# Kernel optimization log

Hardware: AMD Instinct MI355X
Metric: run time of the kernel (lower is better)

## Reference

```python
import jax, jax.numpy as jnp
import numpy as np

B = 4096          # batch_size
D_EMB = 16        # per-side embedding dim (embed_to_from width = 2*D_EMB)
D_HIGH = 784      # flattened high-dim feature size
NSR = 5           # negative_sample_rate
A = 1.576943      # UMAP _a
B_PARAM = 0.8950608  # UMAP _b
REPULSION = 1.0
EPS = 1e-4
GLOBAL_LOSS = 0.5
TOTAL_STEPS = 1000
BATCH_COUNT = 500  # fixed step for deterministic alpha/beta
WARMUP = int(0.05 * TOTAL_STEPS)


def _safe_sqrt(sq):
    # sqrt with zero (not NaN) gradient at 0, matching zero-distance pairs
    safe = jnp.where(sq > 0, sq, 1.0)
    return jnp.where(sq > 0, jnp.sqrt(safe), 0.0)


def _pairwise_dist(x):
    # ||x_i - x_j|| via gram trick; avoids materializing [N,N,D]
    sq = jnp.sum(x * x, axis=1)                      # [N]
    gram = x @ x.T                                   # [N,N]
    d2 = sq[:, None] + sq[None, :] - 2.0 * gram
    return _safe_sqrt(jnp.maximum(d2, 0.0))


def _umap_ce_loss(embed_to_from, perm):
    e_to, e_from = jnp.split(embed_to_from, 2, axis=1)   # [B, D_EMB] each
    neg_to = jnp.repeat(e_to, NSR, axis=0)               # [B*NSR, D_EMB]
    repeat_neg = jnp.repeat(e_from, NSR, axis=0)
    neg_from = repeat_neg[perm]                          # shuffled negatives
    d_pos = _safe_sqrt(jnp.sum((e_to - e_from) ** 2, axis=1))
    d_neg = _safe_sqrt(jnp.sum((neg_to - neg_from) ** 2, axis=1))
    dist = jnp.concatenate([d_pos, d_neg], axis=0)       # [B*(1+NSR)]
    p_dist = 1.0 / (1.0 + A * dist ** (2.0 * B_PARAM))
    p_graph = jnp.concatenate([jnp.ones(B, p_dist.dtype), jnp.zeros(B * NSR, p_dist.dtype)])
    attraction = -p_graph * jnp.log(jnp.clip(p_dist, EPS, 1.0))
    repellant = -(1.0 - p_graph) * jnp.log(jnp.clip(1.0 - p_dist, EPS, 1.0)) * REPULSION
    return jnp.mean(attraction + repellant)


def _global_feature_loss(embed_to_from, to_x):
    e_to = embed_to_from[:, :D_EMB]
    to_x = to_x.reshape(to_x.shape[0], -1)
    high_dis = _pairwise_dist(to_x)     # [N,N]
    low_dis = _pairwise_dist(e_to)      # [N,N]
    # row-wise pearson correlation between high_dis and low_dis
    h = high_dis - jnp.mean(high_dis, axis=1, keepdims=True)
    l = low_dis - jnp.mean(low_dis, axis=1, keepdims=True)
    num = jnp.sum(h * l, axis=1)
    den = jnp.sqrt(jnp.sum(h * h, axis=1)) * jnp.sqrt(jnp.sum(l * l, axis=1))
    corr = jnp.mean(num / den)
    return -corr


def _alpha_beta():
    if BATCH_COUNT >= WARMUP:
        if BATCH_COUNT <= 0.9 * TOTAL_STEPS:
            beta = max(0.0, GLOBAL_LOSS * (1 - BATCH_COUNT / (TOTAL_STEPS - WARMUP * 4)) ** 2)
        else:
            beta = 0.0
        alpha = max(0.0, 1 - beta)
    else:
        alpha = 0.0
        beta = GLOBAL_LOSS
    return alpha, beta


def setup_inputs() -> dict:
    key = jax.random.key(0)
    k1, k2, k3 = jax.random.split(key, 3)
    embed_to_from = jax.random.normal(k1, (B, 2 * D_EMB), dtype=jnp.float32)
    placeholder = jax.random.normal(k2, (B, D_HIGH), dtype=jnp.float32)
    perm = jax.random.permutation(k3, B * NSR).astype(jnp.int32)
    return {"embed_to_from": embed_to_from, "placeholder": placeholder, "perm": perm}


def reference(embed_to_from, placeholder, perm):
    loss = _umap_ce_loss(embed_to_from, perm)
    loss_g = _global_feature_loss(embed_to_from, placeholder)
    alpha, beta = _alpha_beta()
    return alpha * loss + beta * loss_g
```

## Files before the change

### kernel.cpp

```cpp
#include <hip/hip_runtime.h>
#include <hip/hip_bf16.h>
#include <math.h>

#define NB    4096
#define DH    784
#define KX8   832
#define NSR   5
#define NNEG  (NB*NSR)
#define NTOT  (NB + NNEG)

#define A_CONST 1.576943f
#define PEXP    1.7901216f
#define EPS_C   1.0e-4f
#define ALPHA_C 0.9296875f
#define BETA_C  0.0703125f

#define NBLK  528
#define BUFB  8192

typedef __hip_bfloat16 bf16;
typedef short bf16x8 __attribute__((ext_vector_type(8)));
typedef float f32x4  __attribute__((ext_vector_type(4)));
typedef float f32x2  __attribute__((ext_vector_type(2)));
typedef long long2v __attribute__((ext_vector_type(2)));

#define WS_XF8    0
#define WS_EBF    3407872
#define WS_SQX    3670016
#define WS_SQE    3686400
#define WS_ACC5   3702784
#define WS_UPART  8945664
#define WS_CNT    8946304

__device__ __forceinline__ void gl2lds16(const void* g, void* l) {
    __builtin_amdgcn_global_load_lds(
        (const __attribute__((address_space(1))) unsigned int*)g,
        (__attribute__((address_space(3))) unsigned int*)l,
        16, 0, 0);
}

__global__ void prep_fused(const float* __restrict__ X, const float* __restrict__ emb,
                           const int* __restrict__ perm, unsigned char* __restrict__ Xf8,
                           float* __restrict__ sqx, bf16* __restrict__ Ebf,
                           float* __restrict__ sqe, float* __restrict__ upart,
                           float* __restrict__ acc5, unsigned* __restrict__ cnt) {
    if (blockIdx.x == 0 && threadIdx.x == 0) *cnt = 0u;
    if (blockIdx.x < 1024) {
        const int wave = threadIdx.x >> 6, lane = threadIdx.x & 63;
        const int row = blockIdx.x * 4 + wave;
        const float4* xr = (const float4*)(X + (size_t)row * DH);
        int* xb = (int*)(Xf8 + (size_t)row * KX8);
        float s = 0.f;
        #pragma unroll
        for (int it = 0; it < 4; ++it) {
            const int idx = lane + it * 64;
            if (idx < 208) {
                const int c = idx >> 4, p = idx & 15;
                const int q = p >> 2, h = (p >> 1) & 1, w = p & 1;
                const int src = c * 16 + h * 8 + q * 2 + w;
                int pk = 0;
                if (src < 196) {
                    float4 v = xr[src];
                    s += v.x * v.x + v.y * v.y + v.z * v.z + v.w * v.w;
                    int lo = __builtin_amdgcn_cvt_pk_fp8_f32(v.x, v.y, 0, false);
                    pk = __builtin_amdgcn_cvt_pk_fp8_f32(v.z, v.w, lo, true);
                }
                xb[idx] = pk;
            }
        }
        #pragma unroll
        for (int off = 32; off; off >>= 1) s += __shfl_down(s, off, 64);
        if (lane == 0) sqx[row] = s;
        return;
    }
    const int ub = blockIdx.x - 1024;
    const int t = ub * 256 + threadIdx.x;
    if (t < 5 * NB) acc5[t] = 0.f;
    float val = 0.f;
    if (t < NB) {
        const float4* av = (const float4*)(emb + (size_t)t * 32);
        float4 t0 = av[0], t1 = av[1], t2 = av[2], t3 = av[3];
        float4 f0 = av[4], f1 = av[5], f2 = av[6], f3 = av[7];
        bf16* eb = Ebf + (size_t)t * 32;
        union { bf16 h[4]; ushort4 u; } cv;
        #define ST4(dst, q) cv.h[0]=__float2bfloat16(q.x); cv.h[1]=__float2bfloat16(q.y); \
                            cv.h[2]=__float2bfloat16(q.z); cv.h[3]=__float2bfloat16(q.w); \
                            *(ushort4*)(dst) = cv.u;
        ST4(eb,      t0) ST4(eb + 4,  t1) ST4(eb + 8,  t2) ST4(eb + 12, t3)
        #undef ST4
        ushort4 z = {0, 0, 0, 0};
        *(ushort4*)(eb + 16) = z; *(ushort4*)(eb + 20) = z;
        *(ushort4*)(eb + 24) = z; *(ushort4*)(eb + 28) = z;
        sqe[t] = t0.x*t0.x + t0.y*t0.y + t0.z*t0.z + t0.w*t0.w
               + t1.x*t1.x + t1.y*t1.y + t1.z*t1.z + t1.w*t1.w
               + t2.x*t2.x + t2.y*t2.y + t2.z*t2.z + t2.w*t2.w
               + t3.x*t3.x + t3.y*t3.y + t3.z*t3.z + t3.w*t3.w;
        float d2 = 0.f;
        #define D2(a, b) { float4 df = {a.x-b.x, a.y-b.y, a.z-b.z, a.w-b.w}; \
                           d2 += df.x*df.x + df.y*df.y + df.z*df.z + df.w*df.w; }
        D2(t0, f0) D2(t1, f1) D2(t2, f2) D2(t3, f3)
        #undef D2
        float d = sqrtf(d2);
        float p = 1.f / (1.f + A_CONST * powf(d, PEXP));
        val = -logf(fminf(fmaxf(p, EPS_C), 1.f));
    } else if (t < NTOT) {
        const int k = t - NB;
        const int ti = k / 5;
        const int fi = perm[k] / 5;
        const float4* at = (const float4*)(emb + (size_t)ti * 32);
        const float4* bt = (const float4*)(emb + (size_t)fi * 32 + 16);
        float d2 = 0.f;
        #pragma unroll
        for (int q = 0; q < 4; ++q) {
            float4 a = at[q], b = bt[q];
            float4 df = {a.x-b.x, a.y-b.y, a.z-b.z, a.w-b.w};
            d2 += df.x*df.x + df.y*df.y + df.z*df.z + df.w*df.w;
        }
        float d = sqrtf(d2);
        float p = 1.f / (1.f + A_CONST * powf(d, PEXP));
        val = -logf(fminf(fmaxf(1.f - p, EPS_C), 1.f));
    }
    #pragma unroll
    for (int off = 32; off; off >>= 1) val += __shfl_down(val, off, 64);
    __shared__ float ps[4];
    if ((threadIdx.x & 63) == 0) ps[threadIdx.x >> 6] = val;
    __syncthreads();
    if (threadIdx.x == 0) upart[ub] = ps[0] + ps[1] + ps[2] + ps[3];
}

__global__ __launch_bounds__(512, 4) void gram_kernel(
    const unsigned char* __restrict__ Xf8, const bf16* __restrict__ Ebf,
    const float* __restrict__ sqx, const float* __restrict__ sqe,
    float* __restrict__ acc5, const float* __restrict__ upart,
    unsigned* __restrict__ cnt, float* __restrict__ out) {
    __shared__ __align__(16) unsigned char smem[67584];
    unsigned char* As = smem;
    unsigned char* Bs = smem + 4 * BUFB;
    float* sqxs = (float*)(smem + 65536);
    float* sqes = (float*)(smem + 66560);
    float* scr  = (float*)smem;

#define BARLDS() do { asm volatile("s_waitcnt lgkmcnt(0)" ::: "memory"); \
                      __builtin_amdgcn_s_barrier(); } while (0)

    int bi, bj;
    {
        const int k = blockIdx.x & 7;
        const int idx = blockIdx.x >> 3;
        int g = -1, r = 0;
        if (k < 6) {
            const int SG[6] = {0,0,0,1,1,2}, SH[6] = {1,2,3,2,3,3};
            if (idx < 64) { bi = SG[k]*8 + (idx>>3); bj = SH[k]*8 + (idx&7); }
            else {
                const int DG[6] = {1,0,3,1,3,3};
                const int DR[6] = {32,34,30,34,32,34};
                g = DG[k]; r = DR[k] + (idx - 64);
            }
        } else if (k == 6) {
            if (idx < 34) { g = 0; r = idx; } else { g = 1; r = idx - 34; }
        } else {
            if (idx < 36) { g = 2; r = idx; } else { g = 3; r = idx - 36; }
        }
        if (g >= 0) {
            int a = 0;
            while (r >= 8 - a) { r -= 8 - a; ++a; }
            bi = g * 8 + a; bj = g * 8 + a + r;
        }
    }
    const int i0 = bi * 128, j0 = bj * 128;

    const int tid  = threadIdx.x;
    const int wave = tid >> 6;
    const int lane = tid & 63;
    const int wy = wave >> 1, wx = wave & 1;
    const int quad = lane >> 4, l15 = lane & 15;

    f32x4 acc[2][4];
    #pragma unroll
    for (int a = 0; a < 2; ++a)
        #pragma unroll
        for (int b = 0; b < 4; ++b)
            acc[a][b] = (f32x4){0.f, 0.f, 0.f, 0.f};

    const int rA  = lane >> 2;
    const int gsb = (((lane & 3) ^ ((lane >> 3) & 3))) * 16;
    const unsigned char* gA = Xf8 + (size_t)(i0 + wave * 16 + rA) * KX8 + gsb;
    const unsigned char* gB = Xf8 + (size_t)(j0 + wave * 16 + rA) * KX8 + gsb;

    if (tid < 128) {
        sqxs[tid] = sqx[i0 + tid]; sqxs[128 + tid] = sqx[j0 + tid];
        sqes[tid] = sqe[i0 + tid]; sqes[128 + tid] = sqe[j0 + tid];
    }
    __syncthreads();

    #pragma unroll
    for (int s = 0; s < 3; ++s) {
        gl2lds16(gA, As + s * BUFB + wave * 1024);
        gl2lds16(gB, Bs + s * BUFB + wave * 1024);
        gA += 64; gB += 64;
    }

    const int key = (l15 >> 1) & 3;
    const int boX = ((quad ^ key) << 4);

    #pragma unroll
    for (int t = 0; t < 13; ++t) {
        if (t < 12) { asm volatile("s_waitcnt vmcnt(4)" ::: "memory"); }
        else        { asm volatile("s_waitcnt vmcnt(2)" ::: "memory"); }
        __builtin_amdgcn_s_barrier();
        const int cur = (t & 3) * BUFB;
        const int nb  = ((t + 3) & 3) * BUFB;
        if (t < 10) {
            gl2lds16(gA, As + nb + wave * 1024);
            gl2lds16(gB, Bs + nb + wave * 1024);
            gA += 64; gB += 64;
        } else if (t == 10) {
            gl2lds16((const unsigned char*)(Ebf + (size_t)(i0 + wave * 16 + rA) * 32) + gsb,
                     As + BUFB + wave * 1024);
            gl2lds16((const unsigned char*)(Ebf + (size_t)(j0 + wave * 16 + rA) * 32) + gsb,
                     Bs + BUFB + wave * 1024);
        }
        long2v aF[2], bF[4];
        #pragma unroll
        for (int mi = 0; mi < 2; ++mi)
            aF[mi] = *(const long2v*)&As[cur + (wy * 32 + mi * 16 + l15) * 64 + boX];
        #pragma unroll
        for (int ni = 0; ni < 4; ++ni)
            bF[ni] = *(const long2v*)&Bs[cur + (wx * 64 + ni * 16 + l15) * 64 + boX];
        #pragma unroll
        for (int mi = 0; mi < 2; ++mi)
            #pragma unroll
            for (int ni = 0; ni < 4; ++ni) {
                acc[mi][ni] = __builtin_amdgcn_mfma_f32_16x16x32_fp8_fp8(
                    aF[mi][0], bF[ni][0], acc[mi][ni], 0, 0, 0);
                acc[mi][ni] = __builtin_amdgcn_mfma_f32_16x16x32_fp8_fp8(
                    aF[mi][1], bF[ni][1], acc[mi][ni], 0, 0, 0);
            }
    }
    asm volatile("s_waitcnt vmcnt(0)" ::: "memory");
    __builtin_amdgcn_s_barrier();

    bf16x8 afE[2], bfrE[4];
    #pragma unroll
    for (int mi = 0; mi < 2; ++mi)
        afE[mi] = *(const bf16x8*)&As[BUFB + (wy * 32 + mi * 16 + l15) * 64 + boX];
    #pragma unroll
    for (int ni = 0; ni < 4; ++ni)
        bfrE[ni] = *(const bf16x8*)&Bs[BUFB + (wx * 64 + ni * 16 + l15) * 64 + boX];
    float sqxj[4], sqej[4];
    #pragma unroll
    for (int ni = 0; ni < 4; ++ni) {
        const int jl = wx * 64 + ni * 16 + l15;
        sqxj[ni] = sqxs[128 + jl]; sqej[ni] = sqes[128 + jl];
    }
    BARLDS();

    float cst[4][5];
    #pragma unroll
    for (int ni = 0; ni < 4; ++ni)
        #pragma unroll
        for (int c = 0; c < 5; ++c) cst[ni][c] = 0.f;

    #pragma unroll
    for (int mi = 0; mi < 2; ++mi) {
        f32x4 aE[4];
        #pragma unroll
        for (int ni = 0; ni < 4; ++ni) {
            f32x4 z = (f32x4){0.f, 0.f, 0.f, 0.f};
            aE[ni] = __builtin_amdgcn_mfma_f32_16x16x32_bf16(afE[mi], bfrE[ni], z, 0, 0, 0);
        }
        const int ilb = wy * 32 + mi * 16 + quad * 4;
        float sqxi[4], sqei[4];
        #pragma unroll
        for (int r = 0; r < 4; ++r) { sqxi[r] = sqxs[ilb + r]; sqei[r] = sqes[ilb + r]; }
        float rs[5][4];
        #pragma unroll
        for (int c = 0; c < 5; ++c)
            #pragma unroll
            for (int r = 0; r < 4; ++r) rs[c][r] = 0.f;
        #pragma unroll
        for (int ni = 0; ni < 4; ++ni) {
            const int j = j0 + wx * 64 + ni * 16 + l15;
            #pragma unroll
            for (int r = 0; r < 4; ++r) {
                const int i = i0 + ilb + r;
                float H, L;
                if (i == j) { H = 0.f; L = 0.f; }
                else {
                    float d2  = sqxi[r] + sqxj[ni] - 2.0f * acc[mi][ni][r];
                    H = sqrtf(fmaxf(d2, 0.f));
                    float d2e = sqei[r] + sqej[ni] - 2.0f * aE[ni][r];
                    L = sqrtf(fmaxf(d2e, 0.f));
                }
                rs[0][r] += H; rs[1][r] += H * H; rs[2][r] += L;
                rs[3][r] += L * L; rs[4][r] += H * L;
                cst[ni][0] += H; cst[ni][1] += H * H; cst[ni][2] += L;
                cst[ni][3] += L * L; cst[ni][4] += H * L;
            }
        }
        #pragma unroll
        for (int c = 0; c < 5; ++c)
            #pragma unroll
            for (int r = 0; r < 4; ++r)
                scr[(size_t)((((wx * 5 + c) << 6) + (wy << 4) + (quad << 2) + r)) * 18 + l15]
                    = rs[c][r];
        BARLDS();
        for (int o = tid; o < 320; o += 512) {
            const int c = o >> 6, li = o & 63;
            const float* p0 = scr + (size_t)((c << 6) + li) * 18;
            const float* p1 = scr + (size_t)(((5 + c) << 6) + li) * 18;
            float s = 0.f;
            #pragma unroll
            for (int k = 0; k < 16; k += 2) {
                f32x2 v0 = *(const f32x2*)&p0[k]; s += v0.x + v0.y;
                f32x2 v1 = *(const f32x2*)&p1[k]; s += v1.x + v1.y;
            }
            const int iloc = ((li >> 4) << 5) + mi * 16 + (li & 15);
            unsafeAtomicAdd(&acc5[(size_t)c * NB + (i0 + iloc)], s);
        }
        BARLDS();
    }

    if (bi != bj) {
        #pragma unroll
        for (int ni = 0; ni < 4; ++ni) {
            const int jl = wx * 64 + ni * 16 + l15;
            #pragma unroll
            for (int c = 0; c < 5; ++c)
                scr[(size_t)(c * 128 + jl) * 17 + (wy << 2) + quad] = cst[ni][c];
        }
        BARLDS();
        for (int o = tid; o < 640; o += 512) {
            const int c = o >> 7, j = o & 127;
            const float* p = scr + (size_t)(c * 128 + j) * 17;
            float s = (((p[0] + p[1]) + (p[2] + p[3])) + ((p[4] + p[5]) + (p[6] + p[7])))
                    + (((p[8] + p[9]) + (p[10] + p[11])) + ((p[12] + p[13]) + (p[14] + p[15])));
            unsafeAtomicAdd(&acc5[(size_t)c * NB + (j0 + j)], s);
        }
    }

    __shared__ int lastFlag;
    __syncthreads();
    if (tid == 0) {
        __threadfence();
        lastFlag = (atomicAdd(cnt, 1u) == (unsigned)(NBLK - 1));
    }
    __syncthreads();
    if (lastFlag) {
        __threadfence();
        const float invN = 1.0f / (float)NB;
        float v = 0.f;
        #pragma unroll
        for (int rr = 0; rr < 8; ++rr) {
            const int r = tid + rr * 512;
            const float a  = acc5[0 * NB + r];
            const float b  = acc5[1 * NB + r];
            const float c2 = acc5[2 * NB + r];
            const float d  = acc5[3 * NB + r];
            const float e  = acc5[4 * NB + r];
            float num = e - a * c2 * invN;
            float vh  = fmaxf(b - a * a * invN, 0.f);
            float vl  = fmaxf(d - c2 * c2 * invN, 0.f);
            v += num / (sqrtf(vh) * sqrtf(vl));
        }
        v *= (-BETA_C * invN);
        if (tid < 96) v += upart[tid] * (ALPHA_C / (float)NTOT);
        #pragma unroll
        for (int off = 32; off; off >>= 1) v += __shfl_down(v, off, 64);
        float* fin = (float*)smem;
        __syncthreads();
        if ((tid & 63) == 0) fin[tid >> 6] = v;
        __syncthreads();
        if (tid == 0)
            out[0] = ((fin[0] + fin[1]) + (fin[2] + fin[3]))
                   + ((fin[4] + fin[5]) + (fin[6] + fin[7]));
    }
#undef BARLDS
}

extern "C" void kernel_launch(void* const* d_in, const int* in_sizes, int n_in,
                              void* d_out, int out_size, void* d_ws, size_t ws_size,
                              hipStream_t stream) {
    const float* emb  = (const float*)d_in[0];
    const float* ph   = (const float*)d_in[1];
    const int*   perm = (const int*)d_in[2];
    float* out = (float*)d_out;

    char* ws = (char*)d_ws;
    unsigned char* Xf8 = (unsigned char*)(ws + WS_XF8);
    bf16*  Ebf    = (bf16*) (ws + WS_EBF);
    float* sqx    = (float*)(ws + WS_SQX);
    float* sqe    = (float*)(ws + WS_SQE);
    float* acc5   = (float*)(ws + WS_ACC5);
    float* upart  = (float*)(ws + WS_UPART);
    unsigned* cnt = (unsigned*)(ws + WS_CNT);

    prep_fused<<<1120, 256, 0, stream>>>(ph, emb, perm, Xf8, sqx, Ebf, sqe, upart, acc5, cnt);
    gram_kernel<<<NBLK, 512, 0, stream>>>(Xf8, Ebf, sqx, sqe, acc5, upart, cnt, out);
}
```

Baseline: 111.1 us.

## Replace global-to-LDS async loads with register-staged double buffering

Drops the 4-stage pipeline built on direct global-to-LDS loads and uses a 2-buffer LDS scheme fed from registers, prefetching two K-steps ahead. The embedding fragments are now read straight from global memory instead of going through LDS. LDS use falls from about 66KB to 47KB and launch bounds rise from 4 to 6 blocks, aiming for more resident blocks per CU. The cost is extra VGPRs for the staging registers and explicit LDS stores, plus a shallower prefetch distance that may expose more memory latency.

Result: slower. 132.0 us (+18.9%).

```diff
diff --git a/kernel.cpp b/kernel.cpp
--- a/kernel.cpp
+++ b/kernel.cpp
@@ -31,13 +31,6 @@
 #define WS_ACC5   3702784
 #define WS_UPART  8945664
 #define WS_CNT    8946304
-
-__device__ __forceinline__ void gl2lds16(const void* g, void* l) {
-    __builtin_amdgcn_global_load_lds(
-        (const __attribute__((address_space(1))) unsigned int*)g,
-        (__attribute__((address_space(3))) unsigned int*)l,
-        16, 0, 0);
-}
 
 __global__ void prep_fused(const float* __restrict__ X, const float* __restrict__ emb,
                            const int* __restrict__ perm, unsigned char* __restrict__ Xf8,
@@ -128,20 +121,17 @@
     if (threadIdx.x == 0) upart[ub] = ps[0] + ps[1] + ps[2] + ps[3];
 }
 
-__global__ __launch_bounds__(512, 4) void gram_kernel(
+__global__ __launch_bounds__(512, 6) void gram_kernel(
     const unsigned char* __restrict__ Xf8, const bf16* __restrict__ Ebf,
     const float* __restrict__ sqx, const float* __restrict__ sqe,
     float* __restrict__ acc5, const float* __restrict__ upart,
     unsigned* __restrict__ cnt, float* __restrict__ out) {
-    __shared__ __align__(16) unsigned char smem[67584];
+    __shared__ __align__(16) unsigned char smem[48128];
     unsigned char* As = smem;
-    unsigned char* Bs = smem + 4 * BUFB;
-    float* sqxs = (float*)(smem + 65536);
-    float* sqes = (float*)(smem + 66560);
+    unsigned char* Bs = smem + 2 * BUFB;
     float* scr  = (float*)smem;
-
-#define BARLDS() do { asm volatile("s_waitcnt lgkmcnt(0)" ::: "memory"); \
-                      __builtin_amdgcn_s_barrier(); } while (0)
+    float* sqxs = (float*)(smem + 46080);
+    float* sqes = (float*)(smem + 47104);
 
     int bi, bj;
     {
@@ -186,6 +176,7 @@
     const int gsb = (((lane & 3) ^ ((lane >> 3) & 3))) * 16;
     const unsigned char* gA = Xf8 + (size_t)(i0 + wave * 16 + rA) * KX8 + gsb;
     const unsigned char* gB = Xf8 + (size_t)(j0 + wave * 16 + rA) * KX8 + gsb;
+    const int woff = wave * 1024 + (lane << 4);
 
     if (tid < 128) {
         sqxs[tid] = sqx[i0 + tid]; sqxs[128 + tid] = sqx[j0 + tid];
@@ -193,40 +184,32 @@
     }
     __syncthreads();
 
-    #pragma unroll
-    for (int s = 0; s < 3; ++s) {
-        gl2lds16(gA, As + s * BUFB + wave * 1024);
-        gl2lds16(gB, Bs + s * BUFB + wave * 1024);
-        gA += 64; gB += 64;
-    }
+    long2v aBk[2], bBk[2];
+    aBk[0] = *(const long2v*)(gA);      bBk[0] = *(const long2v*)(gB);
+    aBk[1] = *(const long2v*)(gA + 64); bBk[1] = *(const long2v*)(gB + 64);
+    *(long2v*)(As + woff) = aBk[0];
+    *(long2v*)(Bs + woff) = bBk[0];
 
     const int key = (l15 >> 1) & 3;
     const int boX = ((quad ^ key) << 4);
 
     #pragma unroll
     for (int t = 0; t < 13; ++t) {
-        if (t < 12) { asm volatile("s_waitcnt vmcnt(4)" ::: "memory"); }
-        else        { asm volatile("s_waitcnt vmcnt(2)" ::: "memory"); }
+        asm volatile("s_waitcnt lgkmcnt(0)" ::: "memory");
         __builtin_amdgcn_s_barrier();
-        const int cur = (t & 3) * BUFB;
-        const int nb  = ((t + 3) & 3) * BUFB;
-        if (t < 10) {
-            gl2lds16(gA, As + nb + wave * 1024);
-            gl2lds16(gB, Bs + nb + wave * 1024);
-            gA += 64; gB += 64;
-        } else if (t == 10) {
-            gl2lds16((const unsigned char*)(Ebf + (size_t)(i0 + wave * 16 + rA) * 32) + gsb,
-                     As + BUFB + wave * 1024);
-            gl2lds16((const unsigned char*)(Ebf + (size_t)(j0 + wave * 16 + rA) * 32) + gsb,
-                     Bs + BUFB + wave * 1024);
-        }
+        const unsigned char* bufA = As + (t & 1) * BUFB;
+        const unsigned char* bufB = Bs + (t & 1) * BUFB;
         long2v aF[2], bF[4];
         #pragma unroll
         for (int mi = 0; mi < 2; ++mi)
-            aF[mi] = *(const long2v*)&As[cur + (wy * 32 + mi * 16 + l15) * 64 + boX];
+            aF[mi] = *(const long2v*)(bufA + (wy * 32 + mi * 16 + l15) * 64 + boX);
         #pragma unroll
         for (int ni = 0; ni < 4; ++ni)
-            bF[ni] = *(const long2v*)&Bs[cur + (wx * 64 + ni * 16 + l15) * 64 + boX];
+            bF[ni] = *(const long2v*)(bufB + (wx * 64 + ni * 16 + l15) * 64 + boX);
+        if (t + 2 < 13) {
+            aBk[t & 1] = *(const long2v*)(gA + (t + 2) * 64);
+            bBk[t & 1] = *(const long2v*)(gB + (t + 2) * 64);
+        }
         #pragma unroll
         for (int mi = 0; mi < 2; ++mi)
             #pragma unroll
@@ -236,24 +219,27 @@
                 acc[mi][ni] = __builtin_amdgcn_mfma_f32_16x16x32_fp8_fp8(
                     aF[mi][1], bF[ni][1], acc[mi][ni], 0, 0, 0);
             }
-    }
-    asm volatile("s_waitcnt vmcnt(0)" ::: "memory");
-    __builtin_amdgcn_s_barrier();
-
+        if (t + 1 < 13) {
+            *(long2v*)(As + ((t + 1) & 1) * BUFB + woff) = aBk[(t + 1) & 1];
+            *(long2v*)(Bs + ((t + 1) & 1) * BUFB + woff) = bBk[(t + 1) & 1];
+        }
+    }
+
+    const unsigned char* Eb = (const unsigned char*)Ebf;
     bf16x8 afE[2], bfrE[4];
     #pragma unroll
     for (int mi = 0; mi < 2; ++mi)
-        afE[mi] = *(const bf16x8*)&As[BUFB + (wy * 32 + mi * 16 + l15) * 64 + boX];
+        afE[mi] = *(const bf16x8*)(Eb + (size_t)(i0 + wy * 32 + mi * 16 + l15) * 64 + quad * 16);
     #pragma unroll
     for (int ni = 0; ni < 4; ++ni)
-        bfrE[ni] = *(const bf16x8*)&Bs[BUFB + (wx * 64 + ni * 16 + l15) * 64 + boX];
+        bfrE[ni] = *(const bf16x8*)(Eb + (size_t)(j0 + wx * 64 + ni * 16 + l15) * 64 + quad * 16);
     float sqxj[4], sqej[4];
     #pragma unroll
     for (int ni = 0; ni < 4; ++ni) {
         const int jl = wx * 64 + ni * 16 + l15;
         sqxj[ni] = sqxs[128 + jl]; sqej[ni] = sqes[128 + jl];
     }
-    BARLDS();
+    __syncthreads();
 
     float cst[4][5];
     #pragma unroll
@@ -304,7 +290,7 @@
             for (int r = 0; r < 4; ++r)
                 scr[(size_t)((((wx * 5 + c) << 6) + (wy << 4) + (quad << 2) + r)) * 18 + l15]
                     = rs[c][r];
-        BARLDS();
+        __syncthreads();
         for (int o = tid; o < 320; o += 512) {
             const int c = o >> 6, li = o & 63;
             const float* p0 = scr + (size_t)((c << 6) + li) * 18;
@@ -318,7 +304,7 @@
             const int iloc = ((li >> 4) << 5) + mi * 16 + (li & 15);
             unsafeAtomicAdd(&acc5[(size_t)c * NB + (i0 + iloc)], s);
         }
-        BARLDS();
+        __syncthreads();
     }
 
     if (bi != bj) {
@@ -329,7 +315,7 @@
             for (int c = 0; c < 5; ++c)
                 scr[(size_t)(c * 128 + jl) * 17 + (wy << 2) + quad] = cst[ni][c];
         }
-        BARLDS();
+        __syncthreads();
         for (int o = tid; o < 640; o += 512) {
             const int c = o >> 7, j = o & 127;
             const float* p = scr + (size_t)(c * 128 + j) * 17;
@@ -375,7 +361,6 @@
             out[0] = ((fin[0] + fin[1]) + (fin[2] + fin[3]))
                    + ((fin[4] + fin[5]) + (fin[6] + fin[7]));
     }
-#undef BARLDS
 }
 
 extern "C" void kernel_launch(void* const* d_in, const int* in_sizes, int n_in,
```
